# Kernel tuning notes

Hardware: AMD Instinct MI355X
Metric: run time of the kernel (lower is better)

Reference implementation:

```python
import jax, jax.numpy as jnp
import numpy as np

ALPHA = 1.5
N_ITER = 15


def _tsallis_p(X, alpha):
    # gp_inv(clamp(X, 0)) = clamp(X,0) ** (1/(alpha-1))
    return jnp.clip(X, 0.0, None) ** (1.0 / (alpha - 1.0))


def tsallis_bisect(X, alpha=ALPHA, n_iter=N_ITER):
    # X: [n, d] logits; bisection along dim=1
    d = X.shape[1]
    X = X * (alpha - 1.0)
    max_val = jnp.max(X, axis=1, keepdims=True)
    tau_lo = max_val - 1.0  # gp(1) = 1**(alpha-1) = 1
    tau_hi = max_val - (1.0 / d) ** (alpha - 1.0)
    f_lo = jnp.sum(_tsallis_p(X - tau_lo, alpha), axis=1) - 1.0
    dm = tau_hi - tau_lo
    p_m = None
    for _ in range(n_iter):  # fixed small iteration count
        dm = dm / 2.0
        tau_m = tau_lo + dm
        p_m = _tsallis_p(X - tau_m, alpha)
        f_m = jnp.sum(p_m, axis=1) - 1.0
        mask = (f_m * f_lo >= 0.0)[:, None]
        tau_lo = jnp.where(mask, tau_m, tau_lo)
    return p_m


def setup_inputs() -> dict:
    key = jax.random.key(0)
    k1, k2 = jax.random.split(key)
    n, v = 4096, 32000
    inp = jax.random.normal(k1, (n, v), dtype=jnp.float32)
    target = jax.random.randint(k2, (n,), 0, v, dtype=jnp.int64)
    return {"input": inp, "target": target}


def reference(input, target):
    alpha = ALPHA
    n, d = input.shape
    p_star = tsallis_bisect(input, alpha, N_ITER)  # [n, d]
    loss = (1.0 - jnp.sum(p_star ** alpha, axis=1)) / (alpha * (alpha - 1.0))
    # p_star.scatter_add_(1, target, -1): subtract one-hot of target
    p_minus = p_star.at[jnp.arange(n), target].add(-1.0)
    loss = loss + jnp.einsum('ij,ij->i', p_minus, input)
    # ignore_index = -100 < 0 -> no masking; reduction = elementwise_mean
    return jnp.sum(loss) / float(n)
```

## Files before the change

### kernel.cpp

```cpp
#include <hip/hip_runtime.h>

#define BLOCK 1024
#define NW (BLOCK / 64)
#define CAP 6144

__global__ void zero_out_kernel(float* out) { out[0] = 0.0f; }

__device__ __forceinline__ float block_sum(float v, float* red) {
    #pragma unroll
    for (int off = 32; off; off >>= 1) v += __shfl_down(v, off, 64);
    const int tid = threadIdx.x;
    if ((tid & 63) == 0) red[tid >> 6] = v;
    __syncthreads();
    float s = 0.0f;
    #pragma unroll
    for (int w = 0; w < NW; ++w) s += red[w];
    __syncthreads();
    return s;
}

__device__ __forceinline__ float block_max(float v, float* red) {
    #pragma unroll
    for (int off = 32; off; off >>= 1) v = fmaxf(v, __shfl_down(v, off, 64));
    const int tid = threadIdx.x;
    if ((tid & 63) == 0) red[tid >> 6] = v;
    __syncthreads();
    float s = red[0];
    #pragma unroll
    for (int w = 1; w < NW; ++w) s = fmaxf(s, red[w]);
    __syncthreads();
    return s;
}

__global__ __launch_bounds__(BLOCK, 8) void tsallis_kernel(
    const float* __restrict__ inp, const int* __restrict__ tgt,
    float* __restrict__ out, int d, float inv_n)
{
    __shared__ float cbuf[CAP];
    __shared__ float red[NW];
    __shared__ int sK;

    const int row = blockIdx.x;
    const int tid = threadIdx.x;
    const int lane = tid & 63;
    const size_t rb = (size_t)row * (size_t)d;
    const float4* __restrict__ g4 = (const float4*)(inp + rb);
    const int d4 = d >> 2;

    float raw_t = 0.0f;
    if (tid == 0) { sK = 0; raw_t = inp[rb + (size_t)tgt[row]]; }

    float m = -3.4e38f;
    for (int i = tid; i < d4; i += BLOCK) {
        float4 v = g4[i];
        m = fmaxf(fmaxf(m, fmaxf(v.x, v.y)), fmaxf(v.z, v.w));
    }
    const float maxraw = block_max(m, red);
    const float maxv = 0.5f * maxraw;
    const float lo_raw = maxraw - 2.0f;

    for (int i = tid; i < d4; i += BLOCK) {
        float4 v = g4[i];
        float vv[4] = {v.x, v.y, v.z, v.w};
        #pragma unroll
        for (int j = 0; j < 4; ++j) {
            const bool pred = vv[j] > lo_raw;
            const unsigned long long mask = __ballot(pred);
            if (mask) {
                const int leader = __ffsll(mask) - 1;
                int base = 0;
                if (lane == leader) base = atomicAdd(&sK, __popcll(mask));
                base = __shfl(base, leader, 64);
                if (pred) {
                    const int p = base + __popcll(mask & ((1ull << (unsigned)lane) - 1ull));
                    if (p < CAP) cbuf[p] = 0.5f * vv[j];
                }
            }
        }
    }
    __syncthreads();
    const int K = sK;

    float tau_lo = maxv - 1.0f;
    const float tau_hi = maxv - sqrtf(1.0f / (float)d);
    float dm = tau_hi - tau_lo;
    float SA, SPX;

    if (K <= BLOCK) {
        const float hv = (tid < K) ? cbuf[tid] : -1.0e30f;
        float z = fmaxf(hv - tau_lo, 0.0f);
        const float f_lo = block_sum(z * z, red) - 1.0f;
        #pragma unroll 1
        for (int it = 0; it < 14; ++it) {
            dm *= 0.5f;
            const float tm = tau_lo + dm;
            z = fmaxf(hv - tm, 0.0f);
            const float f_m = block_sum(z * z, red) - 1.0f;
            if (f_m * f_lo >= 0.0f) tau_lo = tm;
        }
        dm *= 0.5f;
        const float tm = tau_lo + dm;
        z = fmaxf(hv - tm, 0.0f);
        const float p = z * z;
        SA  = block_sum(p * z, red);
        SPX = block_sum(p * hv, red);
    } else if (K <= CAP) {
        float s = 0.0f;
        for (int idx = tid; idx < K; idx += BLOCK) { float z = fmaxf(cbuf[idx] - tau_lo, 0.0f); s = fmaf(z, z, s); }
        const float f_lo = block_sum(s, red) - 1.0f;
        #pragma unroll 1
        for (int it = 0; it < 14; ++it) {
            dm *= 0.5f;
            const float tm = tau_lo + dm;
            s = 0.0f;
            for (int idx = tid; idx < K; idx += BLOCK) { float z = fmaxf(cbuf[idx] - tm, 0.0f); s = fmaf(z, z, s); }
            const float f_m = block_sum(s, red) - 1.0f;
            if (f_m * f_lo >= 0.0f) tau_lo = tm;
        }
        dm *= 0.5f;
        const float tm = tau_lo + dm;
        float sa = 0.0f, spx = 0.0f;
        for (int idx = tid; idx < K; idx += BLOCK) {
            const float v = cbuf[idx];
            const float z = fmaxf(v - tm, 0.0f); const float p = z * z;
            sa = fmaf(p, z, sa); spx = fmaf(p, v, spx);
        }
        SA = block_sum(sa, red); SPX = block_sum(spx, red);
    } else {
        float s = 0.0f;
        for (int i = tid; i < d4; i += BLOCK) {
            float4 v = g4[i];
            float z;
            z = fmaxf(0.5f * v.x - tau_lo, 0.0f); s = fmaf(z, z, s);
            z = fmaxf(0.5f * v.y - tau_lo, 0.0f); s = fmaf(z, z, s);
            z = fmaxf(0.5f * v.z - tau_lo, 0.0f); s = fmaf(z, z, s);
            z = fmaxf(0.5f * v.w - tau_lo, 0.0f); s = fmaf(z, z, s);
        }
        const float f_lo = block_sum(s, red) - 1.0f;
        #pragma unroll 1
        for (int it = 0; it < 14; ++it) {
            dm *= 0.5f;
            const float tm = tau_lo + dm;
            s = 0.0f;
            for (int i = tid; i < d4; i += BLOCK) {
                float4 v = g4[i];
                float z;
                z = fmaxf(0.5f * v.x - tm, 0.0f); s = fmaf(z, z, s);
                z = fmaxf(0.5f * v.y - tm, 0.0f); s = fmaf(z, z, s);
                z = fmaxf(0.5f * v.z - tm, 0.0f); s = fmaf(z, z, s);
                z = fmaxf(0.5f * v.w - tm, 0.0f); s = fmaf(z, z, s);
            }
            const float f_m = block_sum(s, red) - 1.0f;
            if (f_m * f_lo >= 0.0f) tau_lo = tm;
        }
        dm *= 0.5f;
        const float tm = tau_lo + dm;
        float sa = 0.0f, spx = 0.0f;
        for (int i = tid; i < d4; i += BLOCK) {
            float4 v = g4[i];
            float vv[4] = {0.5f * v.x, 0.5f * v.y, 0.5f * v.z, 0.5f * v.w};
            #pragma unroll
            for (int j = 0; j < 4; ++j) {
                const float z = fmaxf(vv[j] - tm, 0.0f); const float p = z * z;
                sa = fmaf(p, z, sa); spx = fmaf(p, vv[j], spx);
            }
        }
        SA = block_sum(sa, red); SPX = block_sum(spx, red);
    }

    if (tid == 0) {
        const float loss = (1.0f - SA) * (1.0f / 0.75f) + 2.0f * SPX - raw_t;
        atomicAdd(out, loss * inv_n);
    }
}

extern "C" void kernel_launch(void* const* d_in, const int* in_sizes, int n_in,
                              void* d_out, int out_size, void* d_ws, size_t ws_size,
                              hipStream_t stream) {
    const float* inp = (const float*)d_in[0];
    const int*   tgt = (const int*)d_in[1];
    float*       out = (float*)d_out;
    const int n = in_sizes[1];
    const int d = in_sizes[0] / n;

    zero_out_kernel<<<1, 1, 0, stream>>>(out);
    tsallis_kernel<<<n, BLOCK, 0, stream>>>(inp, tgt, out, d, 1.0f / (float)n);
}
```

Baseline: 777.4 us.

## Fuse max and compaction into one pass with two-stage filter and wave-level bisection

The separate max pass over the row is removed. A first-chunk max gives a provisional threshold, and the full max is computed during the same pass that compacts candidates into shared memory. A second filter against the true max then shrinks the candidate set into a small buffer, and a single wave runs the 15-step bisection with register-held values and shuffle reductions instead of block-wide syncs. The block size is halved. The provisional threshold may let many more candidates through and overflow the buffer, which falls back to the slower paths.

After: 739.9 us. 1.05x faster.

```diff
diff --git a/kernel.cpp b/kernel.cpp
--- a/kernel.cpp
+++ b/kernel.cpp
@@ -1,8 +1,9 @@
 #include <hip/hip_runtime.h>
 
-#define BLOCK 1024
+#define BLOCK 512
 #define NW (BLOCK / 64)
-#define CAP 6144
+#define CAP 8192
+#define FCAP 1024
 
 __global__ void zero_out_kernel(float* out) { out[0] = 0.0f; }
 
@@ -30,15 +31,57 @@
     for (int w = 1; w < NW; ++w) s = fmaxf(s, red[w]);
     __syncthreads();
     return s;
+}
+
+__device__ __forceinline__ float wave_sum(float v) {
+    #pragma unroll
+    for (int off = 32; off; off >>= 1) v += __shfl_xor(v, off, 64);
+    return v;
+}
+
+template <int NR>
+__device__ __forceinline__ void wave_bisect(const float* __restrict__ fbuf, int K,
+                                            float tau_lo, float dm, int lane,
+                                            float& SA, float& SPX) {
+    float hv[NR];
+    #pragma unroll
+    for (int j = 0; j < NR; ++j) {
+        const int idx = lane + (j << 6);
+        hv[j] = (idx < K) ? fbuf[idx] : -1.0e30f;
+    }
+    float s = 0.0f;
+    #pragma unroll
+    for (int j = 0; j < NR; ++j) { float z = fmaxf(hv[j] - tau_lo, 0.0f); s = fmaf(z, z, s); }
+    const float f_lo = wave_sum(s) - 1.0f;
+    #pragma unroll 1
+    for (int it = 0; it < 14; ++it) {
+        dm *= 0.5f;
+        const float tm = tau_lo + dm;
+        s = 0.0f;
+        #pragma unroll
+        for (int j = 0; j < NR; ++j) { float z = fmaxf(hv[j] - tm, 0.0f); s = fmaf(z, z, s); }
+        const float f_m = wave_sum(s) - 1.0f;
+        if (f_m * f_lo >= 0.0f) tau_lo = tm;
+    }
+    dm *= 0.5f;
+    const float tm = tau_lo + dm;
+    float sa = 0.0f, spx = 0.0f;
+    #pragma unroll
+    for (int j = 0; j < NR; ++j) {
+        const float z = fmaxf(hv[j] - tm, 0.0f); const float p = z * z;
+        sa = fmaf(p, z, sa); spx = fmaf(p, hv[j], spx);
+    }
+    SA = wave_sum(sa); SPX = wave_sum(spx);
 }
 
 __global__ __launch_bounds__(BLOCK, 8) void tsallis_kernel(
     const float* __restrict__ inp, const int* __restrict__ tgt,
     float* __restrict__ out, int d, float inv_n)
 {
-    __shared__ float cbuf[CAP];
+    __shared__ float sbuf[CAP];
+    __shared__ float fbuf[FCAP];
     __shared__ float red[NW];
-    __shared__ int sK;
+    __shared__ int sK, sKf;
 
     const int row = blockIdx.x;
     const int tid = threadIdx.x;
@@ -48,85 +91,102 @@
     const int d4 = d >> 2;
 
     float raw_t = 0.0f;
-    if (tid == 0) { sK = 0; raw_t = inp[rb + (size_t)tgt[row]]; }
+    if (tid == 0) { sK = 0; sKf = 0; raw_t = inp[rb + (size_t)tgt[row]]; }
 
     float m = -3.4e38f;
-    for (int i = tid; i < d4; i += BLOCK) {
-        float4 v = g4[i];
+    if (tid < d4) {
+        float4 v = g4[tid];
+        m = fmaxf(fmaxf(v.x, v.y), fmaxf(v.z, v.w));
+    }
+    const float thr = block_max(m, red) - 2.0f;
+
+    m = -3.4e38f;
+    const int iters = (d4 + BLOCK - 1) / BLOCK;
+    for (int t = 0; t < iters; ++t) {
+        const int i = tid + t * BLOCK;
+        const bool inb = i < d4;
+        float4 v;
+        if (inb) v = g4[i]; else { v.x = v.y = v.z = v.w = -3.4e38f; }
         m = fmaxf(fmaxf(m, fmaxf(v.x, v.y)), fmaxf(v.z, v.w));
-    }
-    const float maxraw = block_max(m, red);
-    const float maxv = 0.5f * maxraw;
-    const float lo_raw = maxraw - 2.0f;
-
-    for (int i = tid; i < d4; i += BLOCK) {
-        float4 v = g4[i];
-        float vv[4] = {v.x, v.y, v.z, v.w};
+        const float vv[4] = {v.x, v.y, v.z, v.w};
         #pragma unroll
         for (int j = 0; j < 4; ++j) {
-            const bool pred = vv[j] > lo_raw;
+            const bool pred = vv[j] > thr;
             const unsigned long long mask = __ballot(pred);
             if (mask) {
-                const int leader = __ffsll(mask) - 1;
+                const int leader = __ffsll((long long)mask) - 1;
                 int base = 0;
                 if (lane == leader) base = atomicAdd(&sK, __popcll(mask));
                 base = __shfl(base, leader, 64);
                 if (pred) {
                     const int p = base + __popcll(mask & ((1ull << (unsigned)lane) - 1ull));
-                    if (p < CAP) cbuf[p] = 0.5f * vv[j];
+                    if (p < CAP) sbuf[p] = vv[j];
                 }
             }
         }
     }
-    __syncthreads();
-    const int K = sK;
+    const float maxraw = block_max(m, red);
+    const float maxv = 0.5f * maxraw;
+    const int Ksup = sK;
 
     float tau_lo = maxv - 1.0f;
     const float tau_hi = maxv - sqrtf(1.0f / (float)d);
-    float dm = tau_hi - tau_lo;
+    const float dm0 = tau_hi - tau_lo;
     float SA, SPX;
 
-    if (K <= BLOCK) {
-        const float hv = (tid < K) ? cbuf[tid] : -1.0e30f;
-        float z = fmaxf(hv - tau_lo, 0.0f);
-        const float f_lo = block_sum(z * z, red) - 1.0f;
-        #pragma unroll 1
-        for (int it = 0; it < 14; ++it) {
+    if (Ksup <= CAP) {
+        const float fthr = maxraw - 2.0f;
+        const int fiters = (Ksup + BLOCK - 1) / BLOCK;
+        for (int t = 0; t < fiters; ++t) {
+            const int i = tid + t * BLOCK;
+            const bool inb = i < Ksup;
+            const float v = inb ? sbuf[i] : -3.4e38f;
+            const bool pred = inb && (v > fthr);
+            const unsigned long long mask = __ballot(pred);
+            if (mask) {
+                const int leader = __ffsll((long long)mask) - 1;
+                int base = 0;
+                if (lane == leader) base = atomicAdd(&sKf, __popcll(mask));
+                base = __shfl(base, leader, 64);
+                if (pred) {
+                    const int p = base + __popcll(mask & ((1ull << (unsigned)lane) - 1ull));
+                    if (p < FCAP) fbuf[p] = 0.5f * v;
+                }
+            }
+        }
+        __syncthreads();
+        const int K = sKf;
+
+        if (K <= 512) {
+            wave_bisect<8>(fbuf, K, tau_lo, dm0, lane, SA, SPX);
+        } else if (K <= FCAP) {
+            wave_bisect<16>(fbuf, K, tau_lo, dm0, lane, SA, SPX);
+        } else {
+            float dm = dm0;
+            float s = 0.0f;
+            for (int i = tid; i < Ksup; i += BLOCK) { float z = fmaxf(0.5f * sbuf[i] - tau_lo, 0.0f); s = fmaf(z, z, s); }
+            const float f_lo = block_sum(s, red) - 1.0f;
+            #pragma unroll 1
+            for (int it = 0; it < 14; ++it) {
+                dm *= 0.5f;
+                const float tm = tau_lo + dm;
+                s = 0.0f;
+                for (int i = tid; i < Ksup; i += BLOCK) { float z = fmaxf(0.5f * sbuf[i] - tm, 0.0f); s = fmaf(z, z, s); }
+                const float f_m = block_sum(s, red) - 1.0f;
+                if (f_m * f_lo >= 0.0f) tau_lo = tm;
+            }
             dm *= 0.5f;
             const float tm = tau_lo + dm;
-            z = fmaxf(hv - tm, 0.0f);
-            const float f_m = block_sum(z * z, red) - 1.0f;
-            if (f_m * f_lo >= 0.0f) tau_lo = tm;
-        }
-        dm *= 0.5f;
-        const float tm = tau_lo + dm;
-        z = fmaxf(hv - tm, 0.0f);
-        const float p = z * z;
-        SA  = block_sum(p * z, red);
-        SPX = block_sum(p * hv, red);
-    } else if (K <= CAP) {
-        float s = 0.0f;
-        for (int idx = tid; idx < K; idx += BLOCK) { float z = fmaxf(cbuf[idx] - tau_lo, 0.0f); s = fmaf(z, z, s); }
-        const float f_lo = block_sum(s, red) - 1.0f;
-        #pragma unroll 1
-        for (int it = 0; it < 14; ++it) {
-            dm *= 0.5f;
-            const float tm = tau_lo + dm;
-            s = 0.0f;
-            for (int idx = tid; idx < K; idx += BLOCK) { float z = fmaxf(cbuf[idx] - tm, 0.0f); s = fmaf(z, z, s); }
-            const float f_m = block_sum(s, red) - 1.0f;
-            if (f_m * f_lo >= 0.0f) tau_lo = tm;
-        }
-        dm *= 0.5f;
-        const float tm = tau_lo + dm;
-        float sa = 0.0f, spx = 0.0f;
-        for (int idx = tid; idx < K; idx += BLOCK) {
-            const float v = cbuf[idx];
-            const float z = fmaxf(v - tm, 0.0f); const float p = z * z;
-            sa = fmaf(p, z, sa); spx = fmaf(p, v, spx);
-        }
-        SA = block_sum(sa, red); SPX = block_sum(spx, red);
+            float sa = 0.0f, spx = 0.0f;
+            for (int i = tid; i < Ksup; i += BLOCK) {
+                const float v = 0.5f * sbuf[i];
+                const float z = fmaxf(v - tm, 0.0f); const float p = z * z;
+                sa = fmaf(p, z, sa); spx = fmaf(p, v, spx);
+            }
+            SA = block_sum(sa, red); SPX = block_sum(spx, red);
+        }
     } else {
+        float dm = dm0;
         float s = 0.0f;
         for (int i = tid; i < d4; i += BLOCK) {
             float4 v = g4[i];
@@ -158,7 +218,7 @@
         float sa = 0.0f, spx = 0.0f;
         for (int i = tid; i < d4; i += BLOCK) {
             float4 v = g4[i];
-            float vv[4] = {0.5f * v.x, 0.5f * v.y, 0.5f * v.z, 0.5f * v.w};
+            const float vv[4] = {0.5f * v.x, 0.5f * v.y, 0.5f * v.z, 0.5f * v.w};
             #pragma unroll
             for (int j = 0; j < 4; ++j) {
                 const float z = fmaxf(vv[j] - tm, 0.0f); const float p = z * z;
```
